# Kernel optimization log

Hardware: AMD Instinct MI355X
Metric: run time of the kernel (lower is better)

## Reference

```python
import jax, jax.numpy as jnp
import numpy as np

N = 40000   # nodes
E = 150000  # edges (before self-loops)
G = 128     # graphs in batch
V = 20000   # vocab
D = 512     # embedding/hidden dim
H = 4       # heads (layers 0,1)
C = 128     # per-head channels (H*C = D)


def setup_inputs() -> dict:
    key = jax.random.key(0)
    ks = jax.random.split(key, 64)
    n = lambda i, shp, s=0.05: jax.random.normal(ks[i], shp, dtype=jnp.float32) * s
    inp = {}
    inp['node_ids'] = jax.random.randint(ks[0], (N,), 0, V, dtype=jnp.int32)
    inp['edge_index'] = jax.random.randint(ks[1], (2, E), 0, N, dtype=jnp.int32)
    inp['batch'] = jnp.sort(jax.random.randint(ks[2], (N,), 0, G, dtype=jnp.int32))
    inp['emb'] = n(3, (V, D), 0.02)
    # GAT layer 0: D -> H x C, concat
    inp['W0'] = n(4, (D, H * C)); inp['as0'] = n(5, (H, C)); inp['ad0'] = n(6, (H, C)); inp['b0'] = n(7, (D,), 0.01)
    # GAT layer 1: D -> H x C, concat
    inp['W1'] = n(8, (D, H * C)); inp['as1'] = n(9, (H, C)); inp['ad1'] = n(10, (H, C)); inp['b1'] = n(11, (D,), 0.01)
    inp['W2'] = n(12, (D, D)); inp['as2'] = n(13, (1, D)); inp['ad2'] = n(14, (1, D)); inp['b2'] = n(15, (D,), 0.01)
    # danger head
    inp['dW1'] = n(16, (D, D)); inp['db1'] = n(17, (D,), 0.01)
    inp['dg1'] = 1.0 + n(18, (D,), 0.02); inp['dbt1'] = n(19, (D,), 0.02)
    inp['drm1'] = n(20, (D,), 0.02); inp['drv1'] = jax.random.uniform(ks[21], (D,)) + 0.5
    inp['dW2'] = n(22, (D, D // 2)); inp['db2'] = n(23, (D // 2,), 0.01)
    inp['dg2'] = 1.0 + n(24, (D // 2,), 0.02); inp['dbt2'] = n(25, (D // 2,), 0.02)
    inp['drm2'] = n(26, (D // 2,), 0.02); inp['drv2'] = jax.random.uniform(ks[27], (D // 2,)) + 0.5
    inp['dW3'] = n(28, (D // 2, 1)); inp['db3'] = n(29, (1,), 0.01)
    # synergy head
    inp['sW1'] = n(30, (D, D)); inp['sb1'] = n(31, (D,), 0.01)
    inp['sg1'] = 1.0 + n(32, (D,), 0.02); inp['sbt1'] = n(33, (D,), 0.02)
    inp['srm1'] = n(34, (D,), 0.02); inp['srv1'] = jax.random.uniform(ks[35], (D,)) + 0.5
    inp['sW2'] = n(36, (D, D // 2)); inp['sb2'] = n(37, (D // 2,), 0.01)
    inp['sg2'] = 1.0 + n(38, (D // 2,), 0.02); inp['sbt2'] = n(39, (D // 2,), 0.02)
    inp['srm2'] = n(40, (D // 2,), 0.02); inp['srv2'] = jax.random.uniform(ks[41], (D // 2,)) + 0.5
    inp['sW3'] = n(42, (D // 2, 1)); inp['sb3'] = n(43, (1,), 0.01)
    return inp


def _gat(x, W, a_src, a_dst, bias, src, dst, heads, ch, concat):
    # PyG GATConv (eval): linear, per-head additive attention, softmax over
    # incoming edges per destination node, scatter-add aggregate.
    n_nodes = x.shape[0]
    h = (x @ W).reshape(n_nodes, heads, ch)              # [N,H,C]
    e_s = jnp.sum(h * a_src, axis=-1)                    # [N,H]
    e_d = jnp.sum(h * a_dst, axis=-1)                    # [N,H]
    e = jax.nn.leaky_relu(e_s[src] + e_d[dst], 0.2)      # [E,H]
    m = jax.ops.segment_max(e, dst, num_segments=n_nodes)
    m = jnp.where(jnp.isfinite(m), m, 0.0)
    p = jnp.exp(e - m[dst])
    s = jax.ops.segment_sum(p, dst, num_segments=n_nodes)
    alpha = p / (s[dst] + 1e-16)                         # [E,H]
    out = jax.ops.segment_sum(h[src] * alpha[:, :, None], dst, num_segments=n_nodes)
    out = out.reshape(n_nodes, heads * ch) if concat else out.mean(axis=1)
    return out + bias


def _bn(x, g, b, rm, rv):
    return (x - rm) * jax.lax.rsqrt(rv + 1e-5) * g + b


def _head(p, W1, b1, g1, bt1, rm1, rv1, W2, b2, g2, bt2, rm2, rv2, W3, b3):
    z = jax.nn.relu(_bn(p @ W1 + b1, g1, bt1, rm1, rv1))
    z = jax.nn.relu(_bn(z @ W2 + b2, g2, bt2, rm2, rv2))
    return jax.nn.sigmoid(z @ W3 + b3)


def reference(node_ids, edge_index, batch, emb, W0, as0, ad0, b0, W1, as1, ad1, b1, W2, as2, ad2, b2, dW1, db1, dg1, dbt1, drm1, drv1, dW2, db2, dg2, dbt2, drm2, drv2, dW3, db3, sW1, sb1, sg1, sbt1, srm1, srv1, sW2, sb2, sg2, sbt2, srm2, srv2, sW3, sb3):
    loops = jnp.arange(N, dtype=edge_index.dtype)
    src = jnp.concatenate([edge_index[0], loops])
    dst = jnp.concatenate([edge_index[1], loops])
    x = emb[node_ids]                                    # [N,D]
    # layer 0 (no residual)
    x = jax.nn.relu(_gat(x, W0, as0, ad0, b0, src, dst, H, C, True))
    # layer 1 (+residual)
    x = x + jax.nn.relu(_gat(x, W1, as1, ad1, b1, src, dst, H, C, True))
    # layer 2 (+residual)
    x = x + jax.nn.relu(_gat(x, W2, as2, ad2, b2, src, dst, 1, D, False))
    # global mean pool per graph
    sums = jax.ops.segment_sum(x, batch, num_segments=G)
    cnt = jax.ops.segment_sum(jnp.ones((N,), x.dtype), batch, num_segments=G)
    pooled = sums / jnp.maximum(cnt, 1.0)[:, None]       # [G,D]
    danger = _head(pooled, dW1, db1, dg1, dbt1, drm1, drv1, dW2, db2, dg2, dbt2, drm2, drv2, dW3, db3)
    synergy = _head(pooled, sW1, sb1, sg1, sbt1, srm1, srv1, sW2, sb2, sg2, sbt2, srm2, srv2, sW3, sb3)
    return danger, synergy
```

## Files before the change

kernel.cpp:

```cpp
#include <hip/hip_runtime.h>
#include <hip/hip_bf16.h>
#include <stdint.h>

#define NN 40000
#define EE 150000
#define ET 190000
#define GG 128
#define DD 512
#define VV 20000
#define VP 20480
#define MP 40064
#define WB 192
#define NPB0 10240
#define FB 743
#define CW 32
#define NB8 5000

typedef __hip_bfloat16 bf16;
typedef __attribute__((ext_vector_type(8))) short s16x8;
typedef __attribute__((ext_vector_type(4))) float f32v4;

__device__ __forceinline__ float b2f(bf16 v) { return __bfloat162float(v); }
__device__ __forceinline__ bf16  f2b(float v) { return __float2bfloat16(v); }
__device__ __forceinline__ unsigned f2bu(float v) {
    bf16 b = __float2bfloat16(v);
    return (unsigned)*(unsigned short*)&b;
}
__device__ __forceinline__ float lo16(unsigned u) { return __uint_as_float(u << 16); }
__device__ __forceinline__ float hi16(unsigned u) { return __uint_as_float(u & 0xffff0000u); }
__device__ __forceinline__ float s2f(short s) {
    return __uint_as_float(((unsigned)(unsigned short)s) << 16);
}

__device__ __forceinline__ void gl_lds16(const void* g, void* l) {
    __builtin_amdgcn_global_load_lds(
        (const __attribute__((address_space(1))) unsigned int*)g,
        (__attribute__((address_space(3))) unsigned int*)l, 16, 0, 0);
}

__global__ __launch_bounds__(256) void k_prep(const float* __restrict__ W0,
                                              const float* __restrict__ W1,
                                              const float* __restrict__ W2,
                                              bf16* __restrict__ Wt0,
                                              bf16* __restrict__ Wt1,
                                              bf16* __restrict__ Wt2,
                                              const float4* __restrict__ emb4,
                                              bf16* __restrict__ embb,
                                              const int* __restrict__ esrc,
                                              const int* __restrict__ edst,
                                              int* __restrict__ deg,
                                              int* __restrict__ csrf) {
    __shared__ float tile[64][65];
    int b = blockIdx.x, tid = threadIdx.x;
    if (b < WB) {
        int wi = b >> 6, tl = b & 63;
        const float* W; bf16* Wt;
        if (wi == 0)      { W = W0; Wt = Wt0; }
        else if (wi == 1) { W = W1; Wt = Wt1; }
        else              { W = W2; Wt = Wt2; }
        int n0 = (tl & 7) * 64, k0 = (tl >> 3) * 64;
        int rr = tid >> 4, cc = (tid & 15) * 4;
        #pragma unroll
        for (int i = 0; i < 4; i++) {
            int k = k0 + i * 16 + rr;
            float4 v = *(const float4*)(W + (size_t)k * DD + n0 + cc);
            tile[cc + 0][i * 16 + rr] = v.x;
            tile[cc + 1][i * 16 + rr] = v.y;
            tile[cc + 2][i * 16 + rr] = v.z;
            tile[cc + 3][i * 16 + rr] = v.w;
        }
        __syncthreads();
        #pragma unroll
        for (int i = 0; i < 4; i++) {
            int nl = i * 16 + rr;
            ushort4 o;
            o.x = (unsigned short)f2bu(tile[nl][cc + 0]);
            o.y = (unsigned short)f2bu(tile[nl][cc + 1]);
            o.z = (unsigned short)f2bu(tile[nl][cc + 2]);
            o.w = (unsigned short)f2bu(tile[nl][cc + 3]);
            *(ushort4*)(Wt + (size_t)(n0 + nl) * DD + k0 + cc) = o;
        }
    } else if (b < WB + NPB0) {
        int t = (b - WB) * 256 + tid;
        int v = t >> 7, c = t & 127;
        ushort4 u;
        if (v < VV) {
            float4 x = emb4[(size_t)v * 128 + c];
            u.x = (unsigned short)f2bu(x.x); u.y = (unsigned short)f2bu(x.y);
            u.z = (unsigned short)f2bu(x.z); u.w = (unsigned short)f2bu(x.w);
        } else { u.x = 0; u.y = 0; u.z = 0; u.w = 0; }
        *(ushort4*)(embb + (size_t)v * DD + c * 4) = u;
    } else {
        int e = (b - WB - NPB0) * 256 + tid;
        if (e >= ET) return;
        int dst, src;
        if (e < EE) { dst = edst[e]; src = esrc[e]; }
        else        { dst = e - EE;  src = dst; }
        int slot = atomicAdd(&deg[dst], 1);
        if (slot < CW) csrf[dst * CW + slot] = src;
    }
}

template <int H, int MT>
__global__ __launch_bounds__(512) void k_gemm_mfma(const bf16* __restrict__ A,
                                                   const bf16* __restrict__ Bt,
                                                   bf16* __restrict__ C,
                                                   const float* __restrict__ a_s,
                                                   const float* __restrict__ a_d,
                                                   float* __restrict__ es,
                                                   float* __restrict__ ed) {
    constexpr int K = DD, N = DD;
    constexpr int GNBFk = (MT / 8) * 32;
    __shared__ bf16 smem[4 * 128 * 64];
    bf16* lA0 = smem;
    bf16* lB0 = smem + 8192;
    bf16* lA1 = smem + 16384;
    bf16* lB1 = smem + 24576;
    int tid = threadIdx.x, lane = tid & 63, quad = lane >> 4, l16 = lane & 15;
    int w = tid >> 6;

    int bid = blockIdx.x, mt, nt;
    if (bid >= GNBFk) { int r = bid - GNBFk; mt = (MT & ~7) + (r >> 2); nt = r & 3; }
    else { nt = (bid & 31) >> 3; mt = (bid >> 5) * 8 + (bid & 7); }
    int m0 = mt * 128, n0 = nt * 128;
    int wm = (w & 1) * 64, wn = (w >> 1) * 32;

    int l8 = lane >> 3, c16 = (lane & 7) << 4;
    int scol = c16 ^ (l8 << 4);
    const char* pAg = (const char*)A + (size_t)(m0 + w * 16 + l8) * (K * 2) + scol;
    const char* pBg = (const char*)Bt + (size_t)(n0 + w * 16 + l8) * (K * 2) + scol;
    char* dA0 = (char*)lA0 + w * 2048;
    char* dB0 = (char*)lB0 + w * 2048;
    char* dA1 = (char*)lA1 + w * 2048;
    char* dB1 = (char*)lB1 + w * 2048;

    int aoff[2][4], boff[2][2];
    #pragma unroll
    for (int kk = 0; kk < 2; kk++) {
        #pragma unroll
        for (int i = 0; i < 4; i++) {
            int qb = (kk * 4 + quad) << 4;
            int rowA = wm + i * 16 + l16;
            aoff[kk][i] = rowA * 64 + ((qb ^ ((rowA & 7) << 4)) >> 1);
        }
        #pragma unroll
        for (int j = 0; j < 2; j++) {
            int qb = (kk * 4 + quad) << 4;
            int rowB = wn + j * 16 + l16;
            boff[kk][j] = rowB * 64 + ((qb ^ ((rowB & 7) << 4)) >> 1);
        }
    }

    f32v4 zero = 0;
    f32v4 acc[4][2];
    #pragma unroll
    for (int i = 0; i < 4; i++)
        #pragma unroll
        for (int j = 0; j < 2; j++) acc[i][j] = zero;

    auto stage = [&](int kb, char* dA, char* dB) {
        #pragma unroll
        for (int i = 0; i < 2; i++) {
            gl_lds16(pAg + i * 8192 + kb, dA + i * 1024);
            gl_lds16(pBg + i * 8192 + kb, dB + i * 1024);
        }
    };
    auto compute = [&](const bf16* bA, const bf16* bB) {
        #pragma unroll
        for (int kk = 0; kk < 2; kk++) {
            s16x8 a[4], b[2];
            #pragma unroll
            for (int i = 0; i < 4; i++) a[i] = *(const s16x8*)(bA + aoff[kk][i]);
            #pragma unroll
            for (int j = 0; j < 2; j++) b[j] = *(const s16x8*)(bB + boff[kk][j]);
            #pragma unroll
            for (int i = 0; i < 4; i++)
                #pragma unroll
                for (int j = 0; j < 2; j++)
                    acc[i][j] = __builtin_amdgcn_mfma_f32_16x16x32_bf16(a[i], b[j], acc[i][j], 0, 0, 0);
        }
    };

    stage(0, dA0, dB0);
    __syncthreads();
    #pragma unroll
    for (int k0 = 0; k0 < K; k0 += 128) {
        stage((k0 + 64) * 2, dA1, dB1);
        compute(lA0, lB0);
        __syncthreads();
        if (k0 + 128 < K) stage((k0 + 128) * 2, dA0, dB0);
        compute(lA1, lB1);
        __syncthreads();
    }

    float* asl = (float*)(smem + 8192);
    float* adl = asl + 128;
    if (tid < 128)       asl[tid] = a_s[n0 + tid];
    else if (tid < 256)  adl[tid - 128] = a_d[n0 + tid - 128];

    constexpr int ESTR = 136;
    bf16* ebuf = smem;
    int lrB = (w & 1) * 16 + quad * 4;
    int lr = tid >> 4, cc8 = (tid & 15) * 8;
    int grow = m0 + (lr >> 4) * 64 + (lr & 15);
    #pragma unroll
    for (int i = 0; i < 4; i++) {
        __syncthreads();
        #pragma unroll
        for (int j = 0; j < 2; j++) {
            int col = wn + j * 16 + l16;
            #pragma unroll
            for (int r = 0; r < 4; r++)
                ebuf[(lrB + r) * ESTR + col] = f2b(acc[i][j][r]);
        }
        __syncthreads();
        s16x8 v0 = *(s16x8*)(ebuf + lr * ESTR + cc8);
        float ses = 0.f, sed = 0.f;
        #pragma unroll
        for (int k = 0; k < 8; k++) {
            float x = s2f(v0[k]);
            ses += x * asl[cc8 + k];
            sed += x * adl[cc8 + k];
        }
        #pragma unroll
        for (int off = 1; off < 16; off <<= 1) {
            ses += __shfl_xor(ses, off, 64);
            sed += __shfl_xor(sed, off, 64);
        }
        int row = grow + i * 16;
        if ((tid & 15) == 0) {
            if (H == 4) {
                es[(size_t)row * 4 + nt] = ses;
                ed[(size_t)row * 4 + nt] = sed;
            } else {
                es[(size_t)nt * MP + row] = ses;
                ed[(size_t)nt * MP + row] = sed;
            }
        }
        *(s16x8*)(C + (size_t)row * N + n0 + cc8) = v0;
    }
}

template <int H, bool RES, bool FUSE, bool GI>
__global__ __launch_bounds__(256) void k_gat_aggregate(const bf16* __restrict__ h,
                                                       const float* __restrict__ es,
                                                       const float* __restrict__ ed,
                                                       const int* __restrict__ degv,
                                                       const int* __restrict__ csrf,
                                                       const float* __restrict__ bias,
                                                       bf16* __restrict__ xb,
                                                       const int* __restrict__ batch,
                                                       float* __restrict__ psum,
                                                       float* __restrict__ pp,
                                                       const int* __restrict__ idsmap) {
    __shared__ int   s_src[8][32];
    __shared__ float s_a[8][32 * H];
    __shared__ int   s_deg[8];
    __shared__ int   s_gb[FUSE ? 8 : 1];
    __shared__ int   s_g0;
    __shared__ float s_acc[FUSE ? 4 : 1][FUSE ? 8 : 1][FUSE ? 64 : 1];
    int tid = threadIdx.x, w = tid >> 6, lane = tid & 63;
    int half = lane >> 5, el = lane & 31;
    int nb = blockIdx.x * 8;
    if (FUSE && tid == 0) s_g0 = batch[nb];
    {
        int ln = w * 2 + half;
        int node = nb + ln;
        int deg = degv[node];
        if (deg > CW) deg = CW;
        if (el == 0) {
            s_deg[ln] = deg;
            if (FUSE) s_gb[ln] = batch[node];
        }
        float edl[H];
        if (H == 4) {
            int nd = GI ? idsmap[node] : node;
            #pragma unroll
            for (int hh = 0; hh < H; hh++) edl[hh] = ed[nd * H + hh];
        } else {
            edl[0] = ed[node] + ed[MP + node] + ed[2 * MP + node] + ed[3 * MP + node];
        }
        float e_h[H];
        #pragma unroll
        for (int hh = 0; hh < H; hh++) e_h[hh] = -1e30f;
        if (el < deg) {
            int src = csrf[node * CW + el];
            if (GI) src = idsmap[src];
            s_src[ln][el] = src;
            if (H == 4) {
                float4 e4 = *(const float4*)(es + (size_t)src * 4);
                float t4[4] = {e4.x, e4.y, e4.z, e4.w};
                #pragma unroll
                for (int hh = 0; hh < 4; hh++) {
                    float e = t4[hh] + edl[hh];
                    e_h[hh] = e > 0.f ? e : 0.2f * e;
                }
            } else {
                float esv = es[src] + es[MP + src] + es[2 * MP + src] + es[3 * MP + src];
                float e = esv + edl[0];
                e_h[0] = e > 0.f ? e : 0.2f * e;
            }
        }
        float m[H];
        #pragma unroll
        for (int hh = 0; hh < H; hh++) m[hh] = e_h[hh];
        #pragma unroll
        for (int off = 16; off; off >>= 1)
            #pragma unroll
            for (int hh = 0; hh < H; hh++) m[hh] = fmaxf(m[hh], __shfl_xor(m[hh], off, 64));
        float p[H], sum[H];
        #pragma unroll
        for (int hh = 0; hh < H; hh++) {
            p[hh] = (el < deg) ? __expf(e_h[hh] - m[hh]) : 0.f;
            sum[hh] = p[hh];
        }
        #pragma unroll
        for (int off = 16; off; off >>= 1)
            #pragma unroll
            for (int hh = 0; hh < H; hh++) sum[hh] += __shfl_xor(sum[hh], off, 64);
        if (el < deg)
            #pragma unroll
            for (int hh = 0; hh < H; hh++) s_a[ln][el * H + hh] = p[hh] / (sum[hh] + 1e-16f);
    }
    __syncthreads();

    int dbase = lane * 8;
    int hd = (H == 4) ? (lane >> 4) : 0;
    float4 bi0 = *(const float4*)(bias + dbase);
    float4 bi1 = *(const float4*)(bias + dbase + 4);
    int ln0 = w * 2, ln1 = w * 2 + 1;
    int deg0 = s_deg[ln0], deg1 = s_deg[ln1];
    int dmax = deg0 > deg1 ? deg0 : deg1;
    if (FUSE) {
        #pragma unroll
        for (int k = 0; k < 8; k++) s_acc[w][k][lane] = 0.f;
    }
    float A0[8] = {}, A1[8] = {};
    for (int i = 0; i < dmax; i++) {
        if (i < deg0) {
            uint4 u = *(const uint4*)(h + (size_t)s_src[ln0][i] * DD + dbase);
            float a = s_a[ln0][i * H + hd];
            A0[0] += a * lo16(u.x); A0[1] += a * hi16(u.x);
            A0[2] += a * lo16(u.y); A0[3] += a * hi16(u.y);
            A0[4] += a * lo16(u.z); A0[5] += a * hi16(u.z);
            A0[6] += a * lo16(u.w); A0[7] += a * hi16(u.w);
        }
        if (i < deg1) {
            uint4 u = *(const uint4*)(h + (size_t)s_src[ln1][i] * DD + dbase);
            float a = s_a[ln1][i * H + hd];
            A1[0] += a * lo16(u.x); A1[1] += a * hi16(u.x);
            A1[2] += a * lo16(u.y); A1[3] += a * hi16(u.y);
            A1[4] += a * lo16(u.z); A1[5] += a * hi16(u.z);
            A1[6] += a * lo16(u.w); A1[7] += a * hi16(u.w);
        }
    }
    #pragma unroll
    for (int t = 0; t < 2; t++) {
        float* A = (t == 0) ? A0 : A1;
        int nn = w * 2 + t;
        float v[8];
        v[0] = A[0] + bi0.x; v[1] = A[1] + bi0.y;
        v[2] = A[2] + bi0.z; v[3] = A[3] + bi0.w;
        v[4] = A[4] + bi1.x; v[5] = A[5] + bi1.y;
        v[6] = A[6] + bi1.z; v[7] = A[7] + bi1.w;
        #pragma unroll
        for (int k = 0; k < 8; k++) v[k] = fmaxf(v[k], 0.f);
        size_t base = (size_t)(nb + nn) * DD + dbase;
        if (RES) {
            uint4 u = *(const uint4*)(xb + base);
            v[0] += lo16(u.x); v[1] += hi16(u.x);
            v[2] += lo16(u.y); v[3] += hi16(u.y);
            v[4] += lo16(u.z); v[5] += hi16(u.z);
            v[6] += lo16(u.w); v[7] += hi16(u.w);
        }
        if (FUSE) {
            int gn = s_gb[nn];
            if (gn == s_g0) {
                #pragma unroll
                for (int k = 0; k < 8; k++) s_acc[w][k][lane] += v[k];
            } else {
                #pragma unroll
                for (int k = 0; k < 8; k++)
                    atomicAdd(&psum[(size_t)gn * DD + dbase + k], v[k]);
            }
        } else {
            uint4 o;
            o.x = f2bu(v[0]) | (f2bu(v[1]) << 16);
            o.y = f2bu(v[2]) | (f2bu(v[3]) << 16);
            o.z = f2bu(v[4]) | (f2bu(v[5]) << 16);
            o.w = f2bu(v[6]) | (f2bu(v[7]) << 16);
            *(uint4*)(xb + base) = o;
        }
    }
    if (FUSE) {
        __syncthreads();
        int d = tid << 1;
        float a0 = s_acc[0][d & 7][d >> 3] + s_acc[1][d & 7][d >> 3]
                 + s_acc[2][d & 7][d >> 3] + s_acc[3][d & 7][d >> 3];
        int d1 = d + 1;
        float a1 = s_acc[0][d1 & 7][d1 >> 3] + s_acc[1][d1 & 7][d1 >> 3]
                 + s_acc[2][d1 & 7][d1 >> 3] + s_acc[3][d1 & 7][d1 >> 3];
        float2 o = {a0, a1};
        *(float2*)(pp + (size_t)blockIdx.x * DD + d) = o;
    }
}

__global__ __launch_bounds__(256) void k_pool_red(const int* __restrict__ batch,
                                                  const float* __restrict__ pp,
                                                  float* __restrict__ psum) {
    int g = blockIdx.x;
    __shared__ int s_lo, s_hi;
    if (threadIdx.x == 0) {
        int lo = 0, hi = NB8;
        while (lo < hi) { int mid = (lo + hi) >> 1; if (batch[mid * 8] < g) lo = mid + 1; else hi = mid; }
        s_lo = lo;
        lo = 0; hi = NB8;
        while (lo < hi) { int mid = (lo + hi) >> 1; if (batch[mid * 8] < g + 1) lo = mid + 1; else hi = mid; }
        s_hi = lo;
    }
    __syncthreads();
    int d = threadIdx.x * 2;
    float a0 = 0.f, a1 = 0.f;
    for (int b = s_lo; b < s_hi; b++) {
        float2 v = *(const float2*)(pp + (size_t)b * DD + d);
        a0 += v.x; a1 += v.y;
    }
    psum[(size_t)g * DD + d]     += a0;
    psum[(size_t)g * DD + d + 1] += a1;
}

template <int Din, int Dout, bool FIRST>
__global__ __launch_bounds__(256) void k_head_layer2(const float* __restrict__ inD,
                                                     const float* __restrict__ inS,
                                                     const int* __restrict__ batch,
                                                     const float* __restrict__ Wd, const float* __restrict__ bd,
                                                     const float* __restrict__ gd, const float* __restrict__ btd,
                                                     const float* __restrict__ rmd, const float* __restrict__ rvd,
                                                     const float* __restrict__ Ws, const float* __restrict__ bs_,
                                                     const float* __restrict__ gs, const float* __restrict__ bts,
                                                     const float* __restrict__ rms, const float* __restrict__ rvs,
                                                     float* __restrict__ outD,
                                                     float* __restrict__ outS) {
    const float *in, *W, *b, *ga, *bt, *rm, *rv; float* out;
    if (blockIdx.z == 0) { in = inD; W = Wd; b = bd; ga = gd; bt = btd; rm = rmd; rv = rvd; out = outD; }
    else                 { in = inS; W = Ws; b = bs_; ga = gs; bt = bts; rm = rms; rv = rvs; out = outS; }
    int g = blockIdx.y;
    int tid = threadIdx.x;
    int j = blockIdx.x * 64 + (tid & 63);
    int ks = tid >> 6;
    __shared__ float s_in[Din];
    __shared__ float s_red[256];
    __shared__ float s_inv;
    if (FIRST) {
        if (tid == 0) {
            int lo = 0, hi = NN;
            while (lo < hi) { int mid = (lo + hi) >> 1; if (batch[mid] < g) lo = mid + 1; else hi = mid; }
            int a = lo; lo = 0; hi = NN;
            while (lo < hi) { int mid = (lo + hi) >> 1; if (batch[mid] < g + 1) lo = mid + 1; else hi = mid; }
            s_inv = 1.f / fmaxf((float)(lo - a), 1.f);
        }
        __syncthreads();
        for (int k = tid; k < Din; k += 256) s_in[k] = in[(size_t)g * DD + k] * s_inv;
    } else {
        for (int k = tid; k < Din; k += 256) s_in[k] = in[(size_t)g * Din + k];
    }
    __syncthreads();
    constexpr int KS = Din / 4;
    const float* Wp = W + (size_t)ks * KS * Dout + j;
    float acc = 0.f;
    #pragma unroll 8
    for (int k = 0; k < KS; k++) acc += s_in[ks * KS + k] * Wp[(size_t)k * Dout];
    s_red[tid] = acc;
    __syncthreads();
    if (tid < 64) {
        float s = s_red[tid] + s_red[tid + 64] + s_red[tid + 128] + s_red[tid + 192];
        s += b[j];
        s = (s - rm[j]) * rsqrtf(rv[j] + 1e-5f) * ga[j] + bt[j];
        out[(size_t)g * Dout + j] = s > 0.f ? s : 0.f;
    }
}

__global__ __launch_bounds__(64) void k_head_final2(const float* __restrict__ zD,
                                                    const float* __restrict__ zS,
                                                    const float* __restrict__ W3d, const float* __restrict__ b3d,
                                                    const float* __restrict__ W3s, const float* __restrict__ b3s,
                                                    float* __restrict__ out, int Din) {
    const float* z; const float* W3; const float* b3; float* o;
    if (blockIdx.y == 0) { z = zD; W3 = W3d; b3 = b3d; o = out; }
    else                 { z = zS; W3 = W3s; b3 = b3s; o = out + GG; }
    int g = blockIdx.x, lane = threadIdx.x;
    float s = 0.f;
    for (int k = lane; k < Din; k += 64) s += z[(size_t)g * Din + k] * W3[k];
    #pragma unroll
    for (int off = 32; off; off >>= 1) s += __shfl_xor(s, off, 64);
    if (lane == 0) {
        s += b3[0];
        o[g] = 1.f / (1.f + __expf(-s));
    }
}

extern "C" void kernel_launch(void* const* d_in, const int* in_sizes, int n_in,
                              void* d_out, int out_size, void* d_ws, size_t ws_size,
                              hipStream_t stream) {
    const int*   node_ids = (const int*)d_in[0];
    const int*   ei       = (const int*)d_in[1];
    const int*   batch    = (const int*)d_in[2];
    const float* emb      = (const float*)d_in[3];
    const float* W0  = (const float*)d_in[4],  *as0 = (const float*)d_in[5];
    const float* ad0 = (const float*)d_in[6],  *b0  = (const float*)d_in[7];
    const float* W1  = (const float*)d_in[8],  *as1 = (const float*)d_in[9];
    const float* ad1 = (const float*)d_in[10], *b1  = (const float*)d_in[11];
    const float* W2  = (const float*)d_in[12], *as2 = (const float*)d_in[13];
    const float* ad2 = (const float*)d_in[14], *b2  = (const float*)d_in[15];
    const float* dW1 = (const float*)d_in[16], *db1 = (const float*)d_in[17];
    const float* dg1 = (const float*)d_in[18], *dbt1= (const float*)d_in[19];
    const float* drm1= (const float*)d_in[20], *drv1= (const float*)d_in[21];
    const float* dW2 = (const float*)d_in[22], *db2 = (const float*)d_in[23];
    const float* dg2 = (const float*)d_in[24], *dbt2= (const float*)d_in[25];
    const float* drm2= (const float*)d_in[26], *drv2= (const float*)d_in[27];
    const float* dW3 = (const float*)d_in[28], *db3 = (const float*)d_in[29];
    const float* sW1 = (const float*)d_in[30], *sb1 = (const float*)d_in[31];
    const float* sg1 = (const float*)d_in[32], *sbt1= (const float*)d_in[33];
    const float* srm1= (const float*)d_in[34], *srv1= (const float*)d_in[35];
    const float* sW2 = (const float*)d_in[36], *sb2 = (const float*)d_in[37];
    const float* sg2 = (const float*)d_in[38], *sbt2= (const float*)d_in[39];
    const float* srm2= (const float*)d_in[40], *srv2= (const float*)d_in[41];
    const float* sW3 = (const float*)d_in[42], *sb3 = (const float*)d_in[43];

    const int* esrc = ei;
    const int* edst = ei + EE;

    char* p = (char*)d_ws;
    auto alloc = [&](size_t bytes) { char* r = p; p += (bytes + 255) & ~(size_t)255; return (void*)r; };
    bf16*  xb      = (bf16*)alloc((size_t)MP * DD * 2);
    bf16*  hbuf    = (bf16*)alloc((size_t)MP * DD * 2);
    bf16*  embb    = (bf16*)alloc((size_t)VP * DD * 2);
    bf16*  Wt0     = (bf16*)alloc((size_t)DD * DD * 2);
    bf16*  Wt1     = (bf16*)alloc((size_t)DD * DD * 2);
    bf16*  Wt2     = (bf16*)alloc((size_t)DD * DD * 2);
    float* esed    = (float*)alloc((size_t)6 * MP * 4 * 4);
    float* es0 = esed,              *ed0 = esed + (size_t)MP * 4;
    float* es1 = esed + (size_t)MP * 8,  *ed1 = esed + (size_t)MP * 12;
    float* es2 = esed + (size_t)MP * 16, *ed2 = esed + (size_t)MP * 20;
    int*   deg     = (int*)alloc((size_t)NN * 4);
    int*   csrf    = (int*)alloc((size_t)NN * CW * 4);
    float* psum    = (float*)alloc((size_t)GG * DD * 4);
    float* pp      = (float*)alloc((size_t)NB8 * DD * 4);
    float* z1d     = (float*)alloc((size_t)GG * DD * 4);
    float* z1s     = (float*)alloc((size_t)GG * DD * 4);
    float* z2d     = (float*)alloc((size_t)GG * 256 * 4);
    float* z2s     = (float*)alloc((size_t)GG * 256 * 4);

    hipMemsetAsync(deg, 0, (size_t)NN * 4, stream);
    hipMemsetAsync(psum, 0, (size_t)GG * DD * 4, stream);
    k_prep<<<WB + NPB0 + FB, 256, 0, stream>>>(W0, W1, W2, Wt0, Wt1, Wt2,
                                               (const float4*)emb, embb,
                                               esrc, edst, deg, csrf);

    k_gemm_mfma<4, VP / 128><<<(VP / 128) * 4, 512, 0, stream>>>(embb, Wt0, hbuf, as0, ad0, es0, ed0);
    k_gat_aggregate<4, false, false, true><<<NB8, 256, 0, stream>>>(hbuf, es0, ed0, deg, csrf, b0, xb, nullptr, nullptr, nullptr, node_ids);

    k_gemm_mfma<4, MP / 128><<<(MP / 128) * 4, 512, 0, stream>>>(xb, Wt1, hbuf, as1, ad1, es1, ed1);
    k_gat_aggregate<4, true, false, false><<<NB8, 256, 0, stream>>>(hbuf, es1, ed1, deg, csrf, b1, xb, nullptr, nullptr, nullptr, nullptr);

    k_gemm_mfma<1, MP / 128><<<(MP / 128) * 4, 512, 0, stream>>>(xb, Wt2, hbuf, as2, ad2, es2, ed2);
    k_gat_aggregate<1, true, true, false><<<NB8, 256, 0, stream>>>(hbuf, es2, ed2, deg, csrf, b2, xb, batch, psum, pp, nullptr);
    k_pool_red<<<GG, 256, 0, stream>>>(batch, pp, psum);

    float* outp = (float*)d_out;
    dim3 h1grid(DD / 64, GG, 2);
    k_head_layer2<DD, DD, true><<<h1grid, 256, 0, stream>>>(psum, psum, batch,
        dW1, db1, dg1, dbt1, drm1, drv1,
        sW1, sb1, sg1, sbt1, srm1, srv1, z1d, z1s);
    dim3 h2grid(256 / 64, GG, 2);
    k_head_layer2<DD, 256, false><<<h2grid, 256, 0, stream>>>(z1d, z1s, batch,
        dW2, db2, dg2, dbt2, drm2, drv2,
        sW2, sb2, sg2, sbt2, srm2, srv2, z2d, z2s);
    dim3 fgrid(GG, 2);
    k_head_final2<<<fgrid, 64, 0, stream>>>(z2d, z2s, dW3, db3, sW3, sb3, outp, 256);
}
```

Before: 441.3 us.

## Batch MLP head layers over 32 graphs with shared-memory weight tiles

Each head layer kernel now computes a 32-graph by 64-output tile per block. It stages weight and input chunks in shared memory so each weight element is read once per 32 graphs instead of once per graph, which cuts redundant global weight traffic in the small head GEMMs. The psum buffer is moved next to deg so one memset clears both and a launch is saved. The change also reduces the number of blocks, which lowers parallelism for these tiny kernels.

```diff
diff --git a/kernel.cpp b/kernel.cpp
--- a/kernel.cpp
+++ b/kernel.cpp
@@ -430,53 +430,76 @@
 }
 
 template <int Din, int Dout, bool FIRST>
-__global__ __launch_bounds__(256) void k_head_layer2(const float* __restrict__ inD,
-                                                     const float* __restrict__ inS,
-                                                     const int* __restrict__ batch,
-                                                     const float* __restrict__ Wd, const float* __restrict__ bd,
-                                                     const float* __restrict__ gd, const float* __restrict__ btd,
-                                                     const float* __restrict__ rmd, const float* __restrict__ rvd,
-                                                     const float* __restrict__ Ws, const float* __restrict__ bs_,
-                                                     const float* __restrict__ gs, const float* __restrict__ bts,
-                                                     const float* __restrict__ rms, const float* __restrict__ rvs,
-                                                     float* __restrict__ outD,
-                                                     float* __restrict__ outS) {
+__global__ __launch_bounds__(256) void k_head_batched(const float* __restrict__ inD,
+                                                      const float* __restrict__ inS,
+                                                      const int* __restrict__ batch,
+                                                      const float* __restrict__ Wd, const float* __restrict__ bd,
+                                                      const float* __restrict__ gd, const float* __restrict__ btd,
+                                                      const float* __restrict__ rmd, const float* __restrict__ rvd,
+                                                      const float* __restrict__ Ws, const float* __restrict__ bs_,
+                                                      const float* __restrict__ gs, const float* __restrict__ bts,
+                                                      const float* __restrict__ rms, const float* __restrict__ rvs,
+                                                      float* __restrict__ outD,
+                                                      float* __restrict__ outS) {
     const float *in, *W, *b, *ga, *bt, *rm, *rv; float* out;
     if (blockIdx.z == 0) { in = inD; W = Wd; b = bd; ga = gd; bt = btd; rm = rmd; rv = rvd; out = outD; }
     else                 { in = inS; W = Ws; b = bs_; ga = gs; bt = bts; rm = rms; rv = rvs; out = outS; }
-    int g = blockIdx.y;
     int tid = threadIdx.x;
-    int j = blockIdx.x * 64 + (tid & 63);
-    int ks = tid >> 6;
-    __shared__ float s_in[Din];
-    __shared__ float s_red[256];
-    __shared__ float s_inv;
+    int j0 = blockIdx.x * 64;
+    int g0 = blockIdx.y * 32;
+    int g  = tid >> 3;
+    int jj = (tid & 7) * 8;
+
+    __shared__ float sW[128][64];
+    __shared__ float sIn[32][129];
+    __shared__ float s_inv[32];
+
     if (FIRST) {
-        if (tid == 0) {
+        if (tid < 32) {
+            int gg = g0 + tid;
             int lo = 0, hi = NN;
-            while (lo < hi) { int mid = (lo + hi) >> 1; if (batch[mid] < g) lo = mid + 1; else hi = mid; }
+            while (lo < hi) { int mid = (lo + hi) >> 1; if (batch[mid] < gg) lo = mid + 1; else hi = mid; }
             int a = lo; lo = 0; hi = NN;
-            while (lo < hi) { int mid = (lo + hi) >> 1; if (batch[mid] < g + 1) lo = mid + 1; else hi = mid; }
-            s_inv = 1.f / fmaxf((float)(lo - a), 1.f);
-        }
-        __syncthreads();
-        for (int k = tid; k < Din; k += 256) s_in[k] = in[(size_t)g * DD + k] * s_inv;
-    } else {
-        for (int k = tid; k < Din; k += 256) s_in[k] = in[(size_t)g * Din + k];
-    }
-    __syncthreads();
-    constexpr int KS = Din / 4;
-    const float* Wp = W + (size_t)ks * KS * Dout + j;
-    float acc = 0.f;
-    #pragma unroll 8
-    for (int k = 0; k < KS; k++) acc += s_in[ks * KS + k] * Wp[(size_t)k * Dout];
-    s_red[tid] = acc;
-    __syncthreads();
-    if (tid < 64) {
-        float s = s_red[tid] + s_red[tid + 64] + s_red[tid + 128] + s_red[tid + 192];
-        s += b[j];
-        s = (s - rm[j]) * rsqrtf(rv[j] + 1e-5f) * ga[j] + bt[j];
-        out[(size_t)g * Dout + j] = s > 0.f ? s : 0.f;
+            while (lo < hi) { int mid = (lo + hi) >> 1; if (batch[mid] < gg + 1) lo = mid + 1; else hi = mid; }
+            s_inv[tid] = 1.f / fmaxf((float)(lo - a), 1.f);
+        }
+        __syncthreads();
+    }
+
+    float acc[8] = {};
+    for (int kc = 0; kc < Din; kc += 128) {
+        __syncthreads();
+        int jl = tid & 63, kq = (tid >> 6) * 32;
+        #pragma unroll
+        for (int r = 0; r < 32; r++)
+            sW[kq + r][jl] = W[(size_t)(kc + kq + r) * Dout + j0 + jl];
+        #pragma unroll
+        for (int s = 0; s < 16; s++) {
+            int idx = s * 256 + tid;
+            int gl = idx >> 7, kl = idx & 127;
+            float v = in[(size_t)(g0 + gl) * Din + kc + kl];
+            if (FIRST) v *= s_inv[gl];
+            sIn[gl][kl] = v;
+        }
+        __syncthreads();
+        #pragma unroll 4
+        for (int k = 0; k < 128; k++) {
+            float s = sIn[g][k];
+            f32v4 w0 = *(f32v4*)&sW[k][jj];
+            f32v4 w1 = *(f32v4*)&sW[k][jj + 4];
+            acc[0] += s * w0[0]; acc[1] += s * w0[1];
+            acc[2] += s * w0[2]; acc[3] += s * w0[3];
+            acc[4] += s * w1[0]; acc[5] += s * w1[1];
+            acc[6] += s * w1[2]; acc[7] += s * w1[3];
+        }
+    }
+    int gg = g0 + g;
+    #pragma unroll
+    for (int t = 0; t < 8; t++) {
+        int j = j0 + jj + t;
+        float sv = acc[t] + b[j];
+        sv = (sv - rm[j]) * rsqrtf(rv[j] + 1e-5f) * ga[j] + bt[j];
+        out[(size_t)gg * Dout + j] = sv > 0.f ? sv : 0.f;
     }
 }
 
@@ -543,16 +566,15 @@
     float* es1 = esed + (size_t)MP * 8,  *ed1 = esed + (size_t)MP * 12;
     float* es2 = esed + (size_t)MP * 16, *ed2 = esed + (size_t)MP * 20;
     int*   deg     = (int*)alloc((size_t)NN * 4);
+    float* psum    = (float*)alloc((size_t)GG * DD * 4);
     int*   csrf    = (int*)alloc((size_t)NN * CW * 4);
-    float* psum    = (float*)alloc((size_t)GG * DD * 4);
     float* pp      = (float*)alloc((size_t)NB8 * DD * 4);
     float* z1d     = (float*)alloc((size_t)GG * DD * 4);
     float* z1s     = (float*)alloc((size_t)GG * DD * 4);
     float* z2d     = (float*)alloc((size_t)GG * 256 * 4);
     float* z2s     = (float*)alloc((size_t)GG * 256 * 4);
 
-    hipMemsetAsync(deg, 0, (size_t)NN * 4, stream);
-    hipMemsetAsync(psum, 0, (size_t)GG * DD * 4, stream);
+    hipMemsetAsync(deg, 0, (size_t)NN * 4 + (size_t)GG * DD * 4, stream);
     k_prep<<<WB + NPB0 + FB, 256, 0, stream>>>(W0, W1, W2, Wt0, Wt1, Wt2,
                                                (const float4*)emb, embb,
                                                esrc, edst, deg, csrf);
@@ -568,12 +590,12 @@
     k_pool_red<<<GG, 256, 0, stream>>>(batch, pp, psum);
 
     float* outp = (float*)d_out;
-    dim3 h1grid(DD / 64, GG, 2);
-    k_head_layer2<DD, DD, true><<<h1grid, 256, 0, stream>>>(psum, psum, batch,
+    dim3 h1grid(DD / 64, GG / 32, 2);
+    k_head_batched<DD, DD, true><<<h1grid, 256, 0, stream>>>(psum, psum, batch,
         dW1, db1, dg1, dbt1, drm1, drv1,
         sW1, sb1, sg1, sbt1, srm1, srv1, z1d, z1s);
-    dim3 h2grid(256 / 64, GG, 2);
-    k_head_layer2<DD, 256, false><<<h2grid, 256, 0, stream>>>(z1d, z1s, batch,
+    dim3 h2grid(256 / 64, GG / 32, 2);
+    k_head_batched<DD, 256, false><<<h2grid, 256, 0, stream>>>(z1d, z1s, batch,
         dW2, db2, dg2, dbt2, drm2, drv2,
         sW2, sb2, sg2, sbt2, srm2, srv2, z2d, z2s);
     dim3 fgrid(GG, 2);
```

Measured after the change: 444.8 us. No clear change (+0.8%).
